# Kernel optimization log

Hardware: AMD Instinct MI355X
Metric: run time of the kernel (lower is better)

The kernel has to match this reference:

```python
import jax, jax.numpy as jnp
import numpy as np

B, N, M = 16, 4096, 1024
INPUT_DIM, COND_DIM = 512, 512
HEADS, DIM_HEAD = 8, 64
HIDDEN = HEADS * DIM_HEAD


def setup_inputs() -> dict:
    key = jax.random.key(0)
    ks = jax.random.split(key, 6)
    x = jax.random.normal(ks[0], (B, INPUT_DIM, N), dtype=jnp.float32)
    c = jax.random.normal(ks[1], (B, COND_DIM, M), dtype=jnp.float32)
    # 1x1 conv weights as [out_ch, in_ch] matrices
    Wq = jax.random.normal(ks[2], (HIDDEN, INPUT_DIM), dtype=jnp.float32) * (INPUT_DIM ** -0.5)
    Wkv = jax.random.normal(ks[3], (2 * HIDDEN, COND_DIM), dtype=jnp.float32) * (COND_DIM ** -0.5)
    Wo = jax.random.normal(ks[4], (INPUT_DIM, HIDDEN), dtype=jnp.float32) * (HIDDEN ** -0.5)
    bo = jax.random.normal(ks[5], (INPUT_DIM,), dtype=jnp.float32) * 0.01
    return {"x": x, "c": c, "Wq": Wq, "Wkv": Wkv, "Wo": Wo, "bo": bo}


def reference(x, c, Wq, Wkv, Wo, bo):
    scale = DIM_HEAD ** -0.5
    # 1x1 convs == channel-mixing matmuls
    q = jnp.einsum('bcn,oc->bon', x, Wq)            # [B, HIDDEN, N]
    kv = jnp.einsum('bcm,oc->bom', c, Wkv)          # [B, 2*HIDDEN, M]
    k, v = jnp.split(kv, 2, axis=1)                 # each [B, HIDDEN, M]
    # split heads: b (h d) n -> b h d n
    q = q.reshape(B, HEADS, DIM_HEAD, N) * scale
    k = k.reshape(B, HEADS, DIM_HEAD, M)
    v = v.reshape(B, HEADS, DIM_HEAD, M)
    # softmax over conditioning sequence dim
    k = jax.nn.softmax(k, axis=-1)
    # context: [B, H, d, e] (dim_head x dim_head)
    context = jnp.einsum('bhdm,bhem->bhde', k, v)
    # out: [B, H, e, N]
    out = jnp.einsum('bhde,bhdn->bhen', context, q)
    out = out.reshape(B, HIDDEN, N)
    return jnp.einsum('bcn,oc->bon', out, Wo) + bo[None, :, None]
```

## Files before the change

kernel.cpp:

```cpp
#include <hip/hip_runtime.h>

#define KDIM 512

typedef __attribute__((ext_vector_type(8))) short bf16x8;
typedef __attribute__((ext_vector_type(4))) float f32x4;
typedef unsigned short u16;
typedef unsigned int u32;

static __device__ __forceinline__ u16 f2bf(float f) {
  u32 u = __builtin_bit_cast(u32, f);
  u32 r = u + 0x7fffu + ((u >> 16) & 1u);
  return (u16)(r >> 16);
}
static __device__ __forceinline__ bf16x8 ld_frag(const u16* p) {
  uint2 lo = *(const uint2*)p;
  uint2 hi = *(const uint2*)(p + 4);
  uint4 u = make_uint4(lo.x, lo.y, hi.x, hi.y);
  return __builtin_bit_cast(bf16x8, u);
}

#define GLOADLDS(g, l) \
  __builtin_amdgcn_global_load_lds( \
      (const __attribute__((address_space(1))) void*)(g), \
      (__attribute__((address_space(3))) void*)(l), 16, 0, 0)

__global__ __launch_bounds__(256) void cvt_f32_bf16(
    const float* __restrict__ src, u16* __restrict__ dst, int n8)
{
  int i = blockIdx.x * 256 + threadIdx.x;
  if (i >= n8) return;
  float4 a = *(const float4*)(src + (long)i * 8);
  float4 b = *(const float4*)(src + (long)i * 8 + 4);
  u32 w0 = (u32)f2bf(a.x) | ((u32)f2bf(a.y) << 16);
  u32 w1 = (u32)f2bf(a.z) | ((u32)f2bf(a.w) << 16);
  u32 w2 = (u32)f2bf(b.x) | ((u32)f2bf(b.y) << 16);
  u32 w3 = (u32)f2bf(b.z) | ((u32)f2bf(b.w) << 16);
  *(uint4*)(dst + (long)i * 8) = make_uint4(w0, w1, w2, w3);
}

#define A0OFF 0
#define A1OFF 16384
#define B0OFF 32768
#define B1OFF 37376

#define T_GLOADA(kt, ab) { _Pragma("unroll") \
  for (int i_ = 0; i_ < 4; ++i_) { \
    int r_ = (i_ * 8 + wv) * 16 + (lane >> 2); \
    int g_ = (lane & 3) ^ ((r_ >> 2) & 3); \
    GLOADLDS(Ab + (long)r_ * KDIM + (kt) + g_ * 8, \
             &lds[(ab) + (i_ * 8 + wv) * 512]); } }

#define T_LOADB(set, kt) { \
  pb##set##a = *(const float4*)(Bb + (long)((kt) + krow)     * ldn + nq * 4); \
  pb##set##b = *(const float4*)(Bb + (long)((kt) + krow + 1) * ldn + nq * 4); }

#define T_STAGEB(set, bb) { \
  float f0_[4] = {pb##set##a.x, pb##set##a.y, pb##set##a.z, pb##set##a.w}; \
  float f1_[4] = {pb##set##b.x, pb##set##b.y, pb##set##b.z, pb##set##b.w}; \
  _Pragma("unroll") for (int j_ = 0; j_ < 4; ++j_) { \
    u32 w_ = (u32)f2bf(f0_[j_]) | ((u32)f2bf(f1_[j_]) << 16); \
    *(u32*)&lds[(bb) + (nq * 4 + j_) * 36 + krow] = w_; } }

#define T_MFMA(ab, bb) { \
  bf16x8 bfr_[4]; \
  _Pragma("unroll") for (int ni_ = 0; ni_ < 4; ++ni_) \
    bfr_[ni_] = ld_frag(&lds[(bb) + (wn * 64 + ni_ * 16 + lrow) * 36 + lkh * 8]); \
  __builtin_amdgcn_s_setprio(1); \
  _Pragma("unroll") for (int mi_ = 0; mi_ < 8; ++mi_) { \
    int r_ = wm * 128 + mi_ * 16 + lrow; \
    bf16x8 af_ = *(const bf16x8*)&lds[(ab) + r_ * 32 + arsel]; \
    _Pragma("unroll") for (int ni_ = 0; ni_ < 4; ++ni_) \
      acc[mi_][ni_] = __builtin_amdgcn_mfma_f32_16x16x32_bf16(af_, bfr_[ni_], acc[mi_][ni_], 0, 0, 0); } \
  __builtin_amdgcn_s_setprio(0); }

template<bool OUT_BF16, bool BIAS, int MT, int NT>
__global__ __launch_bounds__(512, 2) void gemm_t(
    const u16* __restrict__ Ap, long a_bstride,
    const float* __restrict__ Bp, long b_bstride,
    void* __restrict__ Op, long o_bstride,
    const float* __restrict__ bias, int ldn)
{
  __shared__ u16 lds[41984];

  const int d = blockIdx.x;
  const int mt = d % MT;
  const int nt = (d / MT) % NT;
  const int b  = d / (MT * NT);
  const long mtile = (long)mt * 512;
  const long ntile = (long)nt * 128;
  const u16* Ab = Ap + (long)b * a_bstride + mtile * KDIM;
  const float* Bb = Bp + (long)b * b_bstride + ntile;

  const int t = threadIdx.x;
  const int lane = t & 63, wv = t >> 6;
  const int wm = wv >> 1, wn = wv & 1;
  const int lrow = lane & 15, lkh = lane >> 4;
  const int arsel = (lkh ^ ((lrow >> 2) & 3)) * 8;

  const int nq = t & 31;
  const int hi = (t >> 8) & 1;
  const int kq = ((t >> 5) & 7) ^ ((t >> 2) & 7);
  const int krow = kq * 4 + hi * 2;

  f32x4 acc[8][4] = {};
  float4 pb0a, pb0b, pb1a, pb1b;

  T_LOADB(0, 0)
  T_GLOADA(0, A0OFF)
  T_STAGEB(0, B0OFF)
  __syncthreads();

  for (int s2 = 0; s2 < 8; ++s2) {
    const int kt = s2 * 64;
    T_LOADB(1, kt + 32)
    T_GLOADA(kt + 32, A1OFF)
    T_MFMA(A0OFF, B0OFF)
    T_STAGEB(1, B1OFF)
    __syncthreads();
    if (s2 < 7) {
      T_LOADB(0, kt + 64)
      T_GLOADA(kt + 64, A0OFF)
    }
    T_MFMA(A1OFF, B1OFF)
    if (s2 < 7) {
      T_STAGEB(0, B0OFF)
      __syncthreads();
    }
  }

  #pragma unroll
  for (int mi = 0; mi < 8; ++mi) {
    #pragma unroll
    for (int r = 0; r < 4; ++r) {
      long gr = mtile + wm * 128 + mi * 16 + lkh * 4 + r;
      float bv = 0.0f;
      if constexpr (BIAS) bv = bias[gr];
      #pragma unroll
      for (int ni = 0; ni < 4; ++ni) {
        long gc = ntile + wn * 64 + ni * 16 + lrow;
        float v = acc[mi][ni][r] + bv;
        if constexpr (OUT_BF16)
          ((u16*)Op)[(long)b * o_bstride + gr * ldn + gc] = f2bf(v);
        else
          ((float*)Op)[(long)b * o_bstride + gr * ldn + gc] = v;
      }
    }
  }
}

__global__ __launch_bounds__(256, 2) void softmax_context(
    const u16* __restrict__ kv, float* __restrict__ ctx)
{
  constexpr int LDE = 132;
  __shared__ float rowmax[64], rowinv[64];
  __shared__ u16 Ke[64 * LDE];
  __shared__ u16 Vs[64 * LDE];
  __shared__ float pr[64 * 68];

  const int bh = blockIdx.x;
  const u16* Kr = kv + (long)(bh >> 3) * (1024 * 1024) + (long)(bh & 7) * (64 * 1024);
  const u16* Vr = Kr + 512 * 1024;

  const int t = threadIdx.x;
  const int lane = t & 63, wv = t >> 6;
  const int lrow = lane & 15, lkh = lane >> 4;
  const int d4 = t >> 2, q4 = t & 3;

  {
    const u16* row = Kr + d4 * 1024 + q4 * 256;
    float mx = -3e38f;
    for (int i = 0; i < 256; i += 8) {
      uint4 v = *(const uint4*)(row + i);
      u32 ws[4] = {v.x, v.y, v.z, v.w};
      #pragma unroll
      for (int j = 0; j < 4; ++j) {
        mx = fmaxf(mx, __builtin_bit_cast(float, ws[j] << 16));
        mx = fmaxf(mx, __builtin_bit_cast(float, ws[j] & 0xffff0000u));
      }
    }
    mx = fmaxf(mx, __shfl_xor(mx, 1));
    mx = fmaxf(mx, __shfl_xor(mx, 2));
    float s = 0.f;
    for (int i = 0; i < 256; i += 8) {
      uint4 v = *(const uint4*)(row + i);
      u32 ws[4] = {v.x, v.y, v.z, v.w};
      #pragma unroll
      for (int j = 0; j < 4; ++j) {
        s += __expf(__builtin_bit_cast(float, ws[j] << 16) - mx);
        s += __expf(__builtin_bit_cast(float, ws[j] & 0xffff0000u) - mx);
      }
    }
    s += __shfl_xor(s, 1);
    s += __shfl_xor(s, 2);
    if (q4 == 0) { rowmax[d4] = mx; rowinv[d4] = 1.f / s; }
  }
  __syncthreads();

  f32x4 cacc[4][4] = {};

  for (int mc = 0; mc < 8; ++mc) {
    {
      int dd = t >> 2, j = t & 3;
      int m0 = mc * 128 + j * 32;
      float mx = rowmax[dd], inv = rowinv[dd];
      const u16* src = Kr + dd * 1024 + m0;
      u16* dst = &Ke[dd * LDE + j * 32];
      #pragma unroll
      for (int cq = 0; cq < 4; ++cq) {
        uint4 v = *(const uint4*)(src + cq * 8);
        u32 in[4] = {v.x, v.y, v.z, v.w};
        u32 out[4];
        #pragma unroll
        for (int j2 = 0; j2 < 4; ++j2) {
          float lo = __builtin_bit_cast(float, in[j2] << 16);
          float hif = __builtin_bit_cast(float, in[j2] & 0xffff0000u);
          out[j2] = (u32)f2bf(__expf(lo - mx) * inv) |
                    ((u32)f2bf(__expf(hif - mx) * inv) << 16);
        }
        *(uint2*)(dst + cq * 8)     = make_uint2(out[0], out[1]);
        *(uint2*)(dst + cq * 8 + 4) = make_uint2(out[2], out[3]);
      }
      const u16* vsrc = Vr + dd * 1024 + m0;
      u16* vdst = &Vs[dd * LDE + j * 32];
      #pragma unroll
      for (int cq = 0; cq < 4; ++cq) {
        uint4 v = *(const uint4*)(vsrc + cq * 8);
        *(uint2*)(vdst + cq * 8)     = make_uint2(v.x, v.y);
        *(uint2*)(vdst + cq * 8 + 4) = make_uint2(v.z, v.w);
      }
    }
    __syncthreads();
    bf16x8 ka[4], vb[4];
    #pragma unroll
    for (int mi = 0; mi < 4; ++mi)
      ka[mi] = ld_frag(&Ke[(mi * 16 + lrow) * LDE + wv * 32 + lkh * 8]);
    #pragma unroll
    for (int ni = 0; ni < 4; ++ni)
      vb[ni] = ld_frag(&Vs[(ni * 16 + lrow) * LDE + wv * 32 + lkh * 8]);
    #pragma unroll
    for (int mi = 0; mi < 4; ++mi)
      #pragma unroll
      for (int ni = 0; ni < 4; ++ni)
        cacc[mi][ni] = __builtin_amdgcn_mfma_f32_16x16x32_bf16(ka[mi], vb[ni], cacc[mi][ni], 0, 0, 0);
    __syncthreads();
  }

  for (int w = 0; w < 4; ++w) {
    if (wv == w) {
      #pragma unroll
      for (int mi = 0; mi < 4; ++mi)
        #pragma unroll
        for (int ni = 0; ni < 4; ++ni)
          #pragma unroll
          for (int r = 0; r < 4; ++r) {
            float* p = &pr[(mi * 16 + lkh * 4 + r) * 68 + (ni * 16 + lrow)];
            float v = cacc[mi][ni][r];
            if (w == 0) *p = v; else *p += v;
          }
    }
    __syncthreads();
  }
  float* cg = ctx + (long)bh * 4096;
  for (int i = 0; i < 16; ++i) {
    int o = t + i * 256;
    cg[o] = 0.125f * pr[(o >> 6) * 68 + (o & 63)];
  }
}

__global__ __launch_bounds__(256) void compose_u(
    const float* __restrict__ ctx, const float* __restrict__ Wo, u16* __restrict__ U)
{
  __shared__ float cs[16 * 64];
  const int bh = blockIdx.x, dq = blockIdx.y;
  const int b = bh >> 3, h = bh & 7;
  const int t = threadIdx.x;
  const float* cgrp = ctx + (long)bh * 4096 + dq * 16 * 64;
  for (int i = t; i < 1024; i += 256) cs[i] = cgrp[i];
  __syncthreads();
  #pragma unroll
  for (int rep = 0; rep < 2; ++rep) {
    int o = rep * 256 + t;
    const float* wrow = Wo + (long)o * 512 + h * 64;
    float acc[16] = {};
    for (int e = 0; e < 64; ++e) {
      float w = wrow[e];
      #pragma unroll
      for (int dd = 0; dd < 16; ++dd) acc[dd] += w * cs[dd * 64 + e];
    }
    u16* urow = U + (long)b * (512 * 512) + (long)o * 512 + h * 64 + dq * 16;
    #pragma unroll
    for (int dd = 0; dd < 16; ++dd) urow[dd] = f2bf(acc[dd]);
  }
}

extern "C" void kernel_launch(void* const* d_in, const int* in_sizes, int n_in,
                              void* d_out, int out_size, void* d_ws, size_t ws_size,
                              hipStream_t stream)
{
  const float* x   = (const float*)d_in[0];
  const float* c   = (const float*)d_in[1];
  const float* Wq  = (const float*)d_in[2];
  const float* Wkv = (const float*)d_in[3];
  const float* Wo  = (const float*)d_in[4];
  const float* bo  = (const float*)d_in[5];

  char* ws = (char*)d_ws;
  u16*   kv   = (u16*)ws;
  float* ctx  = (float*)(ws + 33554432);
  u16*   U    = (u16*)(ws + 35651584);
  u16*   Weff = (u16*)(ws + 44040192);
  u16*   Wkvb = (u16*)(ws + 44040192);

  cvt_f32_bf16<<<dim3(256), 256, 0, stream>>>(Wkv, Wkvb, 65536);
  gemm_t<true, false, 2, 8><<<dim3(2 * 8 * 16), 512, 0, stream>>>(
      Wkvb, 0, c, 512L * 1024, kv, 1024L * 1024, nullptr, 1024);
  softmax_context<<<dim3(128), 256, 0, stream>>>(kv, ctx);
  compose_u<<<dim3(128, 4), 256, 0, stream>>>(ctx, Wo, U);
  gemm_t<true, false, 1, 4><<<dim3(1 * 4 * 16), 512, 0, stream>>>(
      U, 512L * 512, Wq, 0, Weff, 512L * 512, nullptr, 512);
  gemm_t<false, true, 1, 32><<<dim3(1 * 32 * 16), 512, 0, stream>>>(
      Weff, 512L * 512, x, 512L * 4096, d_out, 512L * 4096, bo, 4096);
}
```

Baseline: 213.1 us.

## Load GEMM A fragments directly from global memory and cluster blocks by batch

```diff
diff --git a/kernel.cpp b/kernel.cpp
--- a/kernel.cpp
+++ b/kernel.cpp
@@ -18,11 +18,6 @@
   uint4 u = make_uint4(lo.x, lo.y, hi.x, hi.y);
   return __builtin_bit_cast(bf16x8, u);
 }
-
-#define GLOADLDS(g, l) \
-  __builtin_amdgcn_global_load_lds( \
-      (const __attribute__((address_space(1))) void*)(g), \
-      (__attribute__((address_space(3))) void*)(l), 16, 0, 0)
 
 __global__ __launch_bounds__(256) void cvt_f32_bf16(
     const float* __restrict__ src, u16* __restrict__ dst, int n8)
@@ -38,54 +33,54 @@
   *(uint4*)(dst + (long)i * 8) = make_uint4(w0, w1, w2, w3);
 }
 
-#define A0OFF 0
-#define A1OFF 16384
-#define B0OFF 32768
-#define B1OFF 37376
-
-#define T_GLOADA(kt, ab) { _Pragma("unroll") \
-  for (int i_ = 0; i_ < 4; ++i_) { \
-    int r_ = (i_ * 8 + wv) * 16 + (lane >> 2); \
-    int g_ = (lane & 3) ^ ((r_ >> 2) & 3); \
-    GLOADLDS(Ab + (long)r_ * KDIM + (kt) + g_ * 8, \
-             &lds[(ab) + (i_ * 8 + wv) * 512]); } }
-
-#define T_LOADB(set, kt) { \
+#define B0OFF 0
+#define B1OFF 4608
+
+#define W_LOADB(set, kt) { \
   pb##set##a = *(const float4*)(Bb + (long)((kt) + krow)     * ldn + nq * 4); \
   pb##set##b = *(const float4*)(Bb + (long)((kt) + krow + 1) * ldn + nq * 4); }
 
-#define T_STAGEB(set, bb) { \
+#define W_STAGEB(set, bb) { \
   float f0_[4] = {pb##set##a.x, pb##set##a.y, pb##set##a.z, pb##set##a.w}; \
   float f1_[4] = {pb##set##b.x, pb##set##b.y, pb##set##b.z, pb##set##b.w}; \
   _Pragma("unroll") for (int j_ = 0; j_ < 4; ++j_) { \
     u32 w_ = (u32)f2bf(f0_[j_]) | ((u32)f2bf(f1_[j_]) << 16); \
     *(u32*)&lds[(bb) + (nq * 4 + j_) * 36 + krow] = w_; } }
 
-#define T_MFMA(ab, bb) { \
+#define W_MFMA(kt, bb) { \
+  bf16x8 af_[8]; \
+  _Pragma("unroll") for (int mi_ = 0; mi_ < 8; ++mi_) \
+    af_[mi_] = *(const bf16x8*)(Aw + (long)(mi_ * 16) * KDIM + (kt)); \
   bf16x8 bfr_[4]; \
   _Pragma("unroll") for (int ni_ = 0; ni_ < 4; ++ni_) \
     bfr_[ni_] = ld_frag(&lds[(bb) + (wn * 64 + ni_ * 16 + lrow) * 36 + lkh * 8]); \
   __builtin_amdgcn_s_setprio(1); \
-  _Pragma("unroll") for (int mi_ = 0; mi_ < 8; ++mi_) { \
-    int r_ = wm * 128 + mi_ * 16 + lrow; \
-    bf16x8 af_ = *(const bf16x8*)&lds[(ab) + r_ * 32 + arsel]; \
+  _Pragma("unroll") for (int mi_ = 0; mi_ < 8; ++mi_) \
     _Pragma("unroll") for (int ni_ = 0; ni_ < 4; ++ni_) \
-      acc[mi_][ni_] = __builtin_amdgcn_mfma_f32_16x16x32_bf16(af_, bfr_[ni_], acc[mi_][ni_], 0, 0, 0); } \
+      acc[mi_][ni_] = __builtin_amdgcn_mfma_f32_16x16x32_bf16(af_[mi_], bfr_[ni_], acc[mi_][ni_], 0, 0, 0); \
   __builtin_amdgcn_s_setprio(0); }
 
-template<bool OUT_BF16, bool BIAS, int MT, int NT>
-__global__ __launch_bounds__(512, 2) void gemm_t(
+template<bool OUT_BF16, bool BIAS, bool CLUST, int MT, int NT>
+__global__ __launch_bounds__(512, 2) void gemm_w(
     const u16* __restrict__ Ap, long a_bstride,
     const float* __restrict__ Bp, long b_bstride,
     void* __restrict__ Op, long o_bstride,
     const float* __restrict__ bias, int ldn)
 {
-  __shared__ u16 lds[41984];
-
-  const int d = blockIdx.x;
-  const int mt = d % MT;
-  const int nt = (d / MT) % NT;
-  const int b  = d / (MT * NT);
+  __shared__ u16 lds[9216];
+
+  int mt, nt, b;
+  if constexpr (CLUST) {
+    const int bx = blockIdx.x;
+    b  = (bx & 7) | ((bx >> 8) << 3);
+    nt = (bx >> 3) & 31;
+    mt = 0;
+  } else {
+    const int d = blockIdx.x;
+    mt = d % MT;
+    nt = (d / MT) % NT;
+    b  = d / (MT * NT);
+  }
   const long mtile = (long)mt * 512;
   const long ntile = (long)nt * 128;
   const u16* Ab = Ap + (long)b * a_bstride + mtile * KDIM;
@@ -95,7 +90,8 @@
   const int lane = t & 63, wv = t >> 6;
   const int wm = wv >> 1, wn = wv & 1;
   const int lrow = lane & 15, lkh = lane >> 4;
-  const int arsel = (lkh ^ ((lrow >> 2) & 3)) * 8;
+
+  const u16* Aw = Ab + (long)(wm * 128 + lrow) * KDIM + lkh * 8;
 
   const int nq = t & 31;
   const int hi = (t >> 8) & 1;
@@ -105,25 +101,21 @@
   f32x4 acc[8][4] = {};
   float4 pb0a, pb0b, pb1a, pb1b;
 
-  T_LOADB(0, 0)
-  T_GLOADA(0, A0OFF)
-  T_STAGEB(0, B0OFF)
+  W_LOADB(0, 0)
+  W_LOADB(1, 32)
+  W_STAGEB(0, B0OFF)
   __syncthreads();
 
   for (int s2 = 0; s2 < 8; ++s2) {
     const int kt = s2 * 64;
-    T_LOADB(1, kt + 32)
-    T_GLOADA(kt + 32, A1OFF)
-    T_MFMA(A0OFF, B0OFF)
-    T_STAGEB(1, B1OFF)
+    if (s2 < 7) W_LOADB(0, kt + 64)
+    W_MFMA(kt, B0OFF)
+    W_STAGEB(1, B1OFF)
     __syncthreads();
+    if (s2 < 7) W_LOADB(1, kt + 96)
+    W_MFMA(kt + 32, B1OFF)
     if (s2 < 7) {
-      T_LOADB(0, kt + 64)
-      T_GLOADA(kt + 64, A0OFF)
-    }
-    T_MFMA(A1OFF, B1OFF)
-    if (s2 < 7) {
-      T_STAGEB(0, B0OFF)
+      W_STAGEB(0, B0OFF)
       __syncthreads();
     }
   }
@@ -312,12 +304,12 @@
   u16*   Wkvb = (u16*)(ws + 44040192);
 
   cvt_f32_bf16<<<dim3(256), 256, 0, stream>>>(Wkv, Wkvb, 65536);
-  gemm_t<true, false, 2, 8><<<dim3(2 * 8 * 16), 512, 0, stream>>>(
+  gemm_w<true, false, false, 2, 8><<<dim3(2 * 8 * 16), 512, 0, stream>>>(
       Wkvb, 0, c, 512L * 1024, kv, 1024L * 1024, nullptr, 1024);
   softmax_context<<<dim3(128), 256, 0, stream>>>(kv, ctx);
   compose_u<<<dim3(128, 4), 256, 0, stream>>>(ctx, Wo, U);
-  gemm_t<true, false, 1, 4><<<dim3(1 * 4 * 16), 512, 0, stream>>>(
+  gemm_w<true, false, false, 1, 4><<<dim3(1 * 4 * 16), 512, 0, stream>>>(
       U, 512L * 512, Wq, 0, Weff, 512L * 512, nullptr, 512);
-  gemm_t<false, true, 1, 32><<<dim3(1 * 32 * 16), 512, 0, stream>>>(
+  gemm_w<false, true, true, 1, 32><<<dim3(512), 512, 0, stream>>>(
       Weff, 512L * 512, x, 512L * 4096, d_out, 512L * 4096, bo, 4096);
 }
```

Result: slower. 255.6 us (+19.9%).
